# Performance work log

Measured on AMD Instinct MI355X. Metric: run time of the kernel, lower is better.

The kernel has to match this reference:

```python
import jax, jax.numpy as jnp
import numpy as np

D_MODEL = 1024
N_HEAD = 16
D_K = D_MODEL // N_HEAD


def setup_inputs() -> dict:
    key = jax.random.key(0)
    ks = jax.random.split(key, 11)
    B, S, D = 2, 2048, D_MODEL
    scale = 1.0 / np.sqrt(D)
    inp = {
        "q": jax.random.normal(ks[0], (B, S, D), jnp.float32),
        "k": jax.random.normal(ks[1], (B, S, D), jnp.float32),
        "v": jax.random.normal(ks[2], (B, S, D), jnp.float32),
        "w_q": jax.random.normal(ks[3], (D, D), jnp.float32) * scale,
        "b_q": jnp.zeros((D,), jnp.float32),
        "w_k": jax.random.normal(ks[4], (D, D), jnp.float32) * scale,
        "b_k": jnp.zeros((D,), jnp.float32),
        "w_v": jax.random.normal(ks[5], (D, D), jnp.float32) * scale,
        "b_v": jnp.zeros((D,), jnp.float32),
        "w_o": jax.random.normal(ks[6], (D, D), jnp.float32) * scale,
        "b_o": jnp.zeros((D,), jnp.float32),
    }
    return inp


def _split_heads(x):
    # torch: chunk(n_head, dim=-1) then cat(dim=0) -> [H*B, S, d_k]
    B, S, D = x.shape
    x = x.reshape(B, S, N_HEAD, D_K)            # contiguous last-dim chunks
    return x.transpose(2, 0, 1, 3).reshape(N_HEAD * B, S, D_K)


def _merge_heads(x, B):
    # torch: chunk(n_head, dim=0) then cat(dim=-1) -> [B, S, D]
    HB, S, dk = x.shape
    x = x.reshape(N_HEAD, B, S, dk).transpose(1, 2, 0, 3)
    return x.reshape(B, S, N_HEAD * dk)


def reference(q, k, v, w_q, b_q, w_k, b_k, w_v, b_v, w_o, b_o):
    B = q.shape[0]
    qh = _split_heads(q @ w_q + b_q)            # [H*B, S, d_k]
    kh = _split_heads(k @ w_k + b_k)
    vh = _split_heads(v @ w_v + b_v)
    # scaled dot-product attention (naive, materializes scores)
    scores = jnp.einsum('bqd,bkd->bqk', qh, kh) / jnp.sqrt(jnp.float32(D_K))
    attn = jax.nn.softmax(scores, axis=-1)
    out = jnp.einsum('bqk,bkd->bqd', attn, vh)  # [H*B, S, d_k]
    out = _merge_heads(out, B)                  # [B, S, D]
    return out @ w_o + b_o
```

## Files before the change

### kernel.cpp

```cpp
#include <hip/hip_runtime.h>
#include <hip/hip_bf16.h>
#include <stdint.h>

#define DEVINL __device__ __forceinline__

typedef __attribute__((ext_vector_type(8))) short bf16x8;
typedef __attribute__((ext_vector_type(4))) short short4v;
typedef __attribute__((ext_vector_type(8))) unsigned short ushort8;
typedef __attribute__((ext_vector_type(4))) float f32x4;
typedef __attribute__((ext_vector_type(16))) float f32x16;

DEVINL unsigned short f2bf(float x) {
  union { float f; uint32_t u; } v; v.f = x;
  uint32_t u = v.u;
  u += 0x7fffu + ((u >> 16) & 1u);
  return (unsigned short)(u >> 16);
}

DEVINL uint32_t pack_bf16x2(float lo, float hi) {
  __hip_bfloat162 bb = __float22bfloat162_rn(make_float2(lo, hi));
  uint32_t r;
  __builtin_memcpy(&r, &bb, 4);
  return r;
}

DEVINL void gload_lds16(const void* g, void* l) {
  __builtin_amdgcn_global_load_lds((const __attribute__((address_space(1))) void*)g,
                                   (__attribute__((address_space(3))) void*)l, 16, 0, 0);
}

#define E2(x) __builtin_amdgcn_exp2f(x)

DEVINL void barrier_raw() {
  asm volatile("" ::: "memory");
  __builtin_amdgcn_s_barrier();
  asm volatile("" ::: "memory");
}
#define WAITVM(N) asm volatile("s_waitcnt vmcnt(" #N ")" ::: "memory")

__global__ void cvt3_f32_bf16(const float* __restrict__ in0, unsigned short* __restrict__ out0,
                              const float* __restrict__ in1, unsigned short* __restrict__ out1,
                              const float* __restrict__ in2, unsigned short* __restrict__ out2,
                              int nper) {
  int nblk = gridDim.x / 3;
  int which = blockIdx.x / nblk;
  int i = ((blockIdx.x % nblk) * blockDim.x + threadIdx.x) * 8;
  if (i >= nper) return;
  const float* in = which == 0 ? in0 : which == 1 ? in1 : in2;
  unsigned short* out = which == 0 ? out0 : which == 1 ? out1 : out2;
  float4 a = *(const float4*)(in + i);
  float4 b = *(const float4*)(in + i + 4);
  ushort8 r;
  r[0] = f2bf(a.x); r[1] = f2bf(a.y); r[2] = f2bf(a.z); r[3] = f2bf(a.w);
  r[4] = f2bf(b.x); r[5] = f2bf(b.y); r[6] = f2bf(b.z); r[7] = f2bf(b.w);
  *(ushort8*)(out + i) = r;
}

__global__ __launch_bounds__(256) void transpose_w4(
    const float* __restrict__ w0, unsigned short* __restrict__ o0,
    const float* __restrict__ w1, unsigned short* __restrict__ o1,
    const float* __restrict__ w2, unsigned short* __restrict__ o2,
    const float* __restrict__ w3, unsigned short* __restrict__ o3) {
  __shared__ float tile[64][65];
  int z = blockIdx.z;
  const float* w = z == 0 ? w0 : z == 1 ? w1 : z == 2 ? w2 : w3;
  unsigned short* wt = z == 0 ? o0 : z == 1 ? o1 : z == 2 ? o2 : o3;
  int k0 = blockIdx.y * 64, n0 = blockIdx.x * 64;
  int t = threadIdx.x;
  for (int i = 0; i < 4; ++i) {
    int r = (t >> 4) + i * 16;
    int c = (t & 15) * 4;
    float4 v = *(const float4*)(w + (size_t)(k0 + r) * 1024 + n0 + c);
    tile[r][c] = v.x; tile[r][c + 1] = v.y; tile[r][c + 2] = v.z; tile[r][c + 3] = v.w;
  }
  __syncthreads();
  for (int i = 0; i < 4; ++i) {
    int rn = (t >> 4) + i * 16;
    int ck = (t & 15) * 4;
    short4v o;
    o[0] = (short)f2bf(tile[ck + 0][rn]);
    o[1] = (short)f2bf(tile[ck + 1][rn]);
    o[2] = (short)f2bf(tile[ck + 2][rn]);
    o[3] = (short)f2bf(tile[ck + 3][rn]);
    *(short4v*)(wt + (size_t)(n0 + rn) * 1024 + k0 + ck) = o;
  }
}

DEVINL void gemm_body(const unsigned short* __restrict__ A,
                      const unsigned short* __restrict__ Bt,
                      const float* __restrict__ bias,
                      void* __restrict__ out, float scale, int mode,
                      int bx, int by) {
  constexpr int K = 1024;
  __shared__ unsigned short Alds[2 * 128 * 32];
  __shared__ unsigned short Blds[2 * 64 * 32];
  int tile_m = bx * 128;
  int tile_n = by * 64;
  int t = threadIdx.x, lane = t & 63, wid = t >> 6;
  int wm = wid >> 1, wn = wid & 1;
  int fr = lane & 15, fq = lane >> 4;
  f32x4 acc[4][2] = {};

  int ga0 = wid * 64 + lane, ga1 = ga0 + 256;
  int gb0 = wid * 64 + lane;
  int ra0 = ga0 >> 2, ca0 = ((ga0 & 3) ^ ((ra0 >> 1) & 3)) * 8;
  int ra1 = ga1 >> 2, ca1 = ((ga1 & 3) ^ ((ra1 >> 1) & 3)) * 8;
  int rb0 = gb0 >> 2, cb0 = ((gb0 & 3) ^ ((rb0 >> 1) & 3)) * 8;
  const unsigned short* Abase = A  + (size_t)tile_m * K;
  const unsigned short* Bbase = Bt + (size_t)tile_n * K;

  int aoff[4], boff[2];
#pragma unroll
  for (int i = 0; i < 4; ++i) {
    int r = wm * 64 + i * 16 + fr;
    aoff[i] = (r * 4 + (fq ^ ((r >> 1) & 3))) * 8;
  }
#pragma unroll
  for (int j = 0; j < 2; ++j) {
    int r = wn * 32 + j * 16 + fr;
    boff[j] = (r * 4 + (fq ^ ((r >> 1) & 3))) * 8;
  }

  auto stage = [&](int nb, int k0) {
    gload_lds16(Abase + (size_t)ra0 * K + k0 + ca0, Alds + nb * 4096 + ga0 * 8);
    gload_lds16(Abase + (size_t)ra1 * K + k0 + ca1, Alds + nb * 4096 + ga1 * 8);
    gload_lds16(Bbase + (size_t)rb0 * K + k0 + cb0, Blds + nb * 2048 + gb0 * 8);
  };
  auto compute = [&](int nb) {
    bf16x8 af[4], bfb[2];
#pragma unroll
    for (int i = 0; i < 4; ++i) af[i] = *(const bf16x8*)(Alds + nb * 4096 + aoff[i]);
#pragma unroll
    for (int j = 0; j < 2; ++j) bfb[j] = *(const bf16x8*)(Blds + nb * 2048 + boff[j]);
#pragma unroll
    for (int i = 0; i < 4; ++i)
#pragma unroll
      for (int j = 0; j < 2; ++j)
        acc[i][j] = __builtin_amdgcn_mfma_f32_16x16x32_bf16(af[i], bfb[j], acc[i][j], 0, 0, 0);
  };

  stage(0, 0);
  stage(1, 32);
  WAITVM(3);
  barrier_raw();
  for (int it = 0; it < 15; ++it) {
    compute(0);
    barrier_raw();
    stage(0, 64 * it + 64);
    WAITVM(3);
    barrier_raw();
    compute(1);
    barrier_raw();
    stage(1, 64 * it + 96);
    WAITVM(3);
    barrier_raw();
  }
  compute(0);
  barrier_raw();
  WAITVM(0);
  barrier_raw();
  compute(1);

#pragma unroll
  for (int i = 0; i < 4; ++i) {
#pragma unroll
    for (int j = 0; j < 2; ++j) {
      int n = tile_n + wn * 32 + j * 16 + fr;
      float bv = bias[n];
      int m0 = tile_m + wm * 64 + i * 16 + fq * 4;
      if (mode == 0) {
        size_t base = (size_t)((n >> 6) * 2 + (m0 >> 11)) * (2048 * 64) + (n & 63);
#pragma unroll
        for (int r = 0; r < 4; ++r)
          ((unsigned short*)out)[base + (size_t)((m0 + r) & 2047) * 64] =
              f2bf((acc[i][j][r] + bv) * scale);
      } else if (mode == 2) {
        size_t base = (size_t)((n >> 6) * 2 + (m0 >> 11)) * (64 * 2048)
                    + (size_t)(n & 63) * 2048 + (m0 & 2047);
        short4v o;
#pragma unroll
        for (int r = 0; r < 4; ++r) o[r] = (short)f2bf(acc[i][j][r] + bv);
        *(short4v*)((unsigned short*)out + base) = o;
      } else {
#pragma unroll
        for (int r = 0; r < 4; ++r)
          ((float*)out)[(size_t)(m0 + r) * 1024 + n] = acc[i][j][r] + bv;
      }
    }
  }
}

__global__ __launch_bounds__(256) void gemm_qkv(
    const unsigned short* __restrict__ Xq, const unsigned short* __restrict__ Xk,
    const unsigned short* __restrict__ Xv,
    const unsigned short* __restrict__ Wtq, const unsigned short* __restrict__ Wtk,
    const unsigned short* __restrict__ Wtv,
    const float* __restrict__ bq, const float* __restrict__ bk,
    const float* __restrict__ bv,
    unsigned short* __restrict__ Qh, unsigned short* __restrict__ Kh,
    unsigned short* __restrict__ Vt, float qscale) {
  int z = blockIdx.z;
  const unsigned short* A  = z == 0 ? Xq : z == 1 ? Xk : Xv;
  const unsigned short* Bt = z == 0 ? Wtq : z == 1 ? Wtk : Wtv;
  const float* bias        = z == 0 ? bq : z == 1 ? bk : bv;
  void* out                = z == 0 ? (void*)Qh : z == 1 ? (void*)Kh : (void*)Vt;
  float scale = z == 0 ? qscale : 1.0f;
  int mode = z == 2 ? 2 : 0;
  gemm_body(A, Bt, bias, out, scale, mode, blockIdx.x, blockIdx.y);
}

__global__ __launch_bounds__(256) void gemm_o(
    const unsigned short* __restrict__ A, const unsigned short* __restrict__ Bt,
    const float* __restrict__ bias, float* __restrict__ out) {
  gemm_body(A, Bt, bias, out, 1.0f, 1, blockIdx.x, blockIdx.y);
}

__global__ __launch_bounds__(256) void attn_fwd(
    const unsigned short* __restrict__ Qh,
    const unsigned short* __restrict__ Kh,
    const unsigned short* __restrict__ Vtg,
    unsigned short* __restrict__ O) {
  constexpr int S = 2048, DK = 64;
  __shared__ unsigned short Klds[2 * 64 * 64];
  __shared__ unsigned short Vlds[2 * 64 * 64];
  __shared__ unsigned short Plds[4 * 32 * 72];

  int wg = blockIdx.x;
  int swz = (wg & 7) * 64 + (wg >> 3);
  int hb = swz >> 4;
  int qt = swz & 15;
  int t = threadIdx.x, lane = t & 63, wid = t >> 6;
  int lq = lane & 31, hi = lane >> 5;
  int q0 = qt * 128;

  const unsigned short* Qb = Qh  + (size_t)hb * S * DK;
  const unsigned short* Kb = Kh  + (size_t)hb * S * DK;
  const unsigned short* Vb = Vtg + (size_t)hb * DK * S;

  bf16x8 qf[4];
#pragma unroll
  for (int kk = 0; kk < 4; ++kk)
    qf[kk] = *(const bf16x8*)(Qb + (size_t)(q0 + wid * 32 + lq) * DK + kk * 16 + hi * 8);

  int g0 = wid * 128 + lane, g1 = g0 + 64;
  int sr0 = g0 >> 3, sc0 = ((g0 & 7) ^ (sr0 & 7)) * 8;
  int sr1 = g1 >> 3, sc1 = ((g1 & 7) ^ (sr1 & 7)) * 8;

  int koff[2][4], voff[2][4];
#pragma unroll
  for (int h2 = 0; h2 < 2; ++h2) {
    int row = 32 * h2 + lq;
#pragma unroll
    for (int kk = 0; kk < 4; ++kk)
      koff[h2][kk] = (row * 8 + ((2 * kk + hi) ^ (row & 7))) * 8;
  }
#pragma unroll
  for (int jt = 0; jt < 2; ++jt) {
    int row = 32 * jt + lq;
#pragma unroll
    for (int ks = 0; ks < 4; ++ks)
      voff[jt][ks] = (row * 8 + ((2 * ks + hi) ^ (row & 7))) * 8;
  }

  unsigned short* Pw = Plds + wid * (32 * 72) + lq * 72;

  auto stage = [&](int nb, int kt) {
    const unsigned short* Ksrc = Kb + (size_t)kt * 64 * DK;
    const unsigned short* Vsrc = Vb + (size_t)kt * 64;
    gload_lds16(Ksrc + sr0 * 64 + sc0, Klds + nb * 4096 + g0 * 8);
    gload_lds16(Ksrc + sr1 * 64 + sc1, Klds + nb * 4096 + g1 * 8);
    gload_lds16(Vsrc + (size_t)sr0 * S + sc0, Vlds + nb * 4096 + g0 * 8);
    gload_lds16(Vsrc + (size_t)sr1 * S + sc1, Vlds + nb * 4096 + g1 * 8);
  };

  float m = -INFINITY, l = 0.f;
  f32x16 oacc[2] = {};

  auto tilestep = [&](int nb) {
    const unsigned short* Kc = Klds + nb * 4096;
    const unsigned short* Vc = Vlds + nb * 4096;

    f32x16 sacc[2] = {};
#pragma unroll
    for (int kk = 0; kk < 4; ++kk) {
      bf16x8 k0 = *(const bf16x8*)(Kc + koff[0][kk]);
      sacc[0] = __builtin_amdgcn_mfma_f32_32x32x16_bf16(k0, qf[kk], sacc[0], 0, 0, 0);
      bf16x8 k1 = *(const bf16x8*)(Kc + koff[1][kk]);
      sacc[1] = __builtin_amdgcn_mfma_f32_32x32x16_bf16(k1, qf[kk], sacc[1], 0, 0, 0);
    }

    float pmax = fmaxf(sacc[0][0], sacc[0][1]);
#pragma unroll
    for (int r = 2; r < 16; r += 2) pmax = fmaxf(pmax, fmaxf(sacc[0][r], sacc[0][r + 1]));
#pragma unroll
    for (int r = 0; r < 16; r += 2) pmax = fmaxf(pmax, fmaxf(sacc[1][r], sacc[1][r + 1]));
    pmax = fmaxf(pmax, __shfl_xor(pmax, 32, 64));

    if (!__all(pmax <= m + 8.0f)) {
      float mn = fmaxf(m, pmax);
      float cf = E2(m - mn);
      m = mn;
      l *= cf;
#pragma unroll
      for (int jt = 0; jt < 2; ++jt)
#pragma unroll
        for (int r = 0; r < 16; ++r) oacc[jt][r] *= cf;
    }

    float ps[4] = {0.f, 0.f, 0.f, 0.f};
#pragma unroll
    for (int r = 0; r < 16; ++r) {
      float p0 = E2(sacc[0][r] - m);
      float p1 = E2(sacc[1][r] - m);
      sacc[0][r] = p0; sacc[1][r] = p1;
      ps[r & 3] += p0 + p1;
    }
    float psum = (ps[0] + ps[1]) + (ps[2] + ps[3]);
    psum += __shfl_xor(psum, 32, 64);
    l += psum;

#pragma unroll
    for (int h2 = 0; h2 < 2; ++h2)
#pragma unroll
      for (int rp = 0; rp < 8; ++rp) {
        uint32_t w = pack_bf16x2(sacc[h2][2 * rp], sacc[h2][2 * rp + 1]);
        int key = 32 * h2 + 8 * (rp >> 1) + 4 * hi + 2 * (rp & 1);
        *(uint32_t*)(Pw + key) = w;
      }
    bf16x8 pfrag[4];
#pragma unroll
    for (int ks = 0; ks < 4; ++ks)
      pfrag[ks] = *(const bf16x8*)(Pw + 16 * ks + 8 * hi);

#pragma unroll
    for (int jt = 0; jt < 2; ++jt)
#pragma unroll
      for (int ks = 0; ks < 4; ++ks) {
        bf16x8 vf = *(const bf16x8*)(Vc + voff[jt][ks]);
        oacc[jt] = __builtin_amdgcn_mfma_f32_32x32x16_bf16(vf, pfrag[ks], oacc[jt], 0, 0, 0);
      }
  };

  stage(0, 0);
  stage(1, 1);
  WAITVM(4);
  barrier_raw();
  for (int it = 0; it < 15; ++it) {
    tilestep(0);
    barrier_raw();
    stage(0, 2 * it + 2);
    WAITVM(4);
    barrier_raw();
    tilestep(1);
    barrier_raw();
    stage(1, 2 * it + 3);
    WAITVM(4);
    barrier_raw();
  }
  tilestep(0);
  barrier_raw();
  WAITVM(0);
  barrier_raw();
  tilestep(1);

  int h = hb >> 1, b = hb & 1;
  int q = q0 + wid * 32 + lq;
  float linv = 1.0f / l;
  unsigned short* orow = O + (size_t)(b * 2048 + q) * 1024 + h * 64;
#pragma unroll
  for (int jt = 0; jt < 2; ++jt)
#pragma unroll
    for (int g = 0; g < 4; ++g) {
      short4v o;
#pragma unroll
      for (int r = 0; r < 4; ++r) o[r] = (short)f2bf(oacc[jt][4 * g + r] * linv);
      *(short4v*)(orow + jt * 32 + 8 * g + 4 * hi) = o;
    }
}

extern "C" void kernel_launch(void* const* d_in, const int* in_sizes, int n_in,
                              void* d_out, int out_size, void* d_ws, size_t ws_size,
                              hipStream_t stream) {
  const float* q   = (const float*)d_in[0];
  const float* k   = (const float*)d_in[1];
  const float* v   = (const float*)d_in[2];
  const float* w_q = (const float*)d_in[3];
  const float* b_q = (const float*)d_in[4];
  const float* w_k = (const float*)d_in[5];
  const float* b_k = (const float*)d_in[6];
  const float* w_v = (const float*)d_in[7];
  const float* b_v = (const float*)d_in[8];
  const float* w_o = (const float*)d_in[9];
  const float* b_o = (const float*)d_in[10];

  char* ws = (char*)d_ws;
  unsigned short* Xq  = (unsigned short*)(ws + 0);
  unsigned short* Xk  = (unsigned short*)(ws + 8388608);
  unsigned short* Xv  = (unsigned short*)(ws + 16777216);
  unsigned short* Wtq = (unsigned short*)(ws + 25165824);
  unsigned short* Wtk = (unsigned short*)(ws + 27262976);
  unsigned short* Wtv = (unsigned short*)(ws + 29360128);
  unsigned short* Wto = (unsigned short*)(ws + 31457280);
  unsigned short* Qh  = (unsigned short*)(ws + 33554432);
  unsigned short* Kh  = (unsigned short*)(ws + 41943040);
  unsigned short* Vt  = (unsigned short*)(ws + 50331648);
  unsigned short* Obuf = Xq;

  const int NACT = 4096 * 1024;
  cvt3_f32_bf16<<<3 * (NACT / 8 / 256), 256, 0, stream>>>(q, Xq, k, Xk, v, Xv, NACT);

  dim3 tg(16, 16, 4);
  transpose_w4<<<tg, 256, 0, stream>>>(w_q, Wtq, w_k, Wtk, w_v, Wtv, w_o, Wto);

  const float qscale = 0.125f * 1.44269504088896340736f;
  dim3 gq(32, 16, 3);
  gemm_qkv<<<gq, 256, 0, stream>>>(Xq, Xk, Xv, Wtq, Wtk, Wtv,
                                   b_q, b_k, b_v, Qh, Kh, Vt, qscale);

  attn_fwd<<<512, 256, 0, stream>>>(Qh, Kh, Vt, Obuf);

  dim3 gg(32, 16);
  gemm_o<<<gg, 256, 0, stream>>>(Obuf, Wto, b_o, (float*)d_out);
}
```

Measured before the change: 146.2 us.

## Build P fragments in registers via permuted V layout, drop P LDS round-trip

The V-projection GEMM epilogue now writes V^T with a permuted key order, so the softmax probabilities in the score accumulator can be packed directly into MFMA operand fragments without a trip through LDS. The attention loop is restructured to issue the next tile's loads before computing the current one, using __syncthreads instead of explicit vmcnt waits. It also raises wave priority around the MFMA blocks. Correctness depends on the permutation matching between the V layout and the P fragment order, and the synchronization change alters how much load latency is hidden.

```diff
diff --git a/kernel.cpp b/kernel.cpp
--- a/kernel.cpp
+++ b/kernel.cpp
@@ -9,6 +9,7 @@
 typedef __attribute__((ext_vector_type(8))) unsigned short ushort8;
 typedef __attribute__((ext_vector_type(4))) float f32x4;
 typedef __attribute__((ext_vector_type(16))) float f32x16;
+typedef __attribute__((ext_vector_type(4))) int int4v;
 
 DEVINL unsigned short f2bf(float x) {
   union { float f; uint32_t u; } v; v.f = x;
@@ -17,9 +18,9 @@
   return (unsigned short)(u >> 16);
 }
 
-DEVINL uint32_t pack_bf16x2(float lo, float hi) {
+DEVINL int pack_bf16x2(float lo, float hi) {
   __hip_bfloat162 bb = __float22bfloat162_rn(make_float2(lo, hi));
-  uint32_t r;
+  int r;
   __builtin_memcpy(&r, &bb, 4);
   return r;
 }
@@ -161,6 +162,7 @@
   barrier_raw();
   compute(1);
 
+  int fqs = ((fq & 1) << 1) | (fq >> 1);
 #pragma unroll
   for (int i = 0; i < 4; ++i) {
 #pragma unroll
@@ -175,8 +177,9 @@
           ((unsigned short*)out)[base + (size_t)((m0 + r) & 2047) * 64] =
               f2bf((acc[i][j][r] + bv) * scale);
       } else if (mode == 2) {
+        int m0s = tile_m + wm * 64 + i * 16 + fqs * 4;
         size_t base = (size_t)((n >> 6) * 2 + (m0 >> 11)) * (64 * 2048)
-                    + (size_t)(n & 63) * 2048 + (m0 & 2047);
+                    + (size_t)(n & 63) * 2048 + (m0s & 2047);
         short4v o;
 #pragma unroll
         for (int r = 0; r < 4; ++r) o[r] = (short)f2bf(acc[i][j][r] + bv);
@@ -223,7 +226,6 @@
   constexpr int S = 2048, DK = 64;
   __shared__ unsigned short Klds[2 * 64 * 64];
   __shared__ unsigned short Vlds[2 * 64 * 64];
-  __shared__ unsigned short Plds[4 * 32 * 72];
 
   int wg = blockIdx.x;
   int swz = (wg & 7) * 64 + (wg >> 3);
@@ -261,8 +263,6 @@
     for (int ks = 0; ks < 4; ++ks)
       voff[jt][ks] = (row * 8 + ((2 * ks + hi) ^ (row & 7))) * 8;
   }
-
-  unsigned short* Pw = Plds + wid * (32 * 72) + lq * 72;
 
   auto stage = [&](int nb, int kt) {
     const unsigned short* Ksrc = Kb + (size_t)kt * 64 * DK;
@@ -281,6 +281,7 @@
     const unsigned short* Vc = Vlds + nb * 4096;
 
     f32x16 sacc[2] = {};
+    __builtin_amdgcn_s_setprio(1);
 #pragma unroll
     for (int kk = 0; kk < 4; ++kk) {
       bf16x8 k0 = *(const bf16x8*)(Kc + koff[0][kk]);
@@ -288,6 +289,7 @@
       bf16x8 k1 = *(const bf16x8*)(Kc + koff[1][kk]);
       sacc[1] = __builtin_amdgcn_mfma_f32_32x32x16_bf16(k1, qf[kk], sacc[1], 0, 0, 0);
     }
+    __builtin_amdgcn_s_setprio(0);
 
     float pmax = fmaxf(sacc[0][0], sacc[0][1]);
 #pragma unroll
@@ -319,19 +321,19 @@
     psum += __shfl_xor(psum, 32, 64);
     l += psum;
 
-#pragma unroll
-    for (int h2 = 0; h2 < 2; ++h2)
-#pragma unroll
-      for (int rp = 0; rp < 8; ++rp) {
-        uint32_t w = pack_bf16x2(sacc[h2][2 * rp], sacc[h2][2 * rp + 1]);
-        int key = 32 * h2 + 8 * (rp >> 1) + 4 * hi + 2 * (rp & 1);
-        *(uint32_t*)(Pw + key) = w;
-      }
     bf16x8 pfrag[4];
 #pragma unroll
-    for (int ks = 0; ks < 4; ++ks)
-      pfrag[ks] = *(const bf16x8*)(Pw + 16 * ks + 8 * hi);
-
+    for (int ks = 0; ks < 4; ++ks) {
+      const int h2 = ks >> 1, b = 8 * (ks & 1);
+      int4v w;
+      w[0] = pack_bf16x2(sacc[h2][b + 0], sacc[h2][b + 1]);
+      w[1] = pack_bf16x2(sacc[h2][b + 2], sacc[h2][b + 3]);
+      w[2] = pack_bf16x2(sacc[h2][b + 4], sacc[h2][b + 5]);
+      w[3] = pack_bf16x2(sacc[h2][b + 6], sacc[h2][b + 7]);
+      pfrag[ks] = __builtin_bit_cast(bf16x8, w);
+    }
+
+    __builtin_amdgcn_s_setprio(1);
 #pragma unroll
     for (int jt = 0; jt < 2; ++jt)
 #pragma unroll
@@ -339,29 +341,20 @@
         bf16x8 vf = *(const bf16x8*)(Vc + voff[jt][ks]);
         oacc[jt] = __builtin_amdgcn_mfma_f32_32x32x16_bf16(vf, pfrag[ks], oacc[jt], 0, 0, 0);
       }
+    __builtin_amdgcn_s_setprio(0);
   };
 
   stage(0, 0);
-  stage(1, 1);
-  WAITVM(4);
-  barrier_raw();
-  for (int it = 0; it < 15; ++it) {
+  __syncthreads();
+  for (int it = 0; it < 16; ++it) {
+    int t1 = 2 * it + 1, t2 = 2 * it + 2;
+    stage(1, t1);
     tilestep(0);
-    barrier_raw();
-    stage(0, 2 * it + 2);
-    WAITVM(4);
-    barrier_raw();
+    __syncthreads();
+    if (t2 < 32) stage(0, t2);
     tilestep(1);
-    barrier_raw();
-    stage(1, 2 * it + 3);
-    WAITVM(4);
-    barrier_raw();
-  }
-  tilestep(0);
-  barrier_raw();
-  WAITVM(0);
-  barrier_raw();
-  tilestep(1);
+    __syncthreads();
+  }
 
   int h = hb >> 1, b = hb & 1;
   int q = q0 + wid * 32 + lq;
```

Result: no change. 143.7 us (-1.7%).
